# Kernel optimization log

Hardware: AMD Instinct MI355X
Metric: run time of the kernel (lower is better)

The kernel has to match this reference:

```python
import jax, jax.numpy as jnp
import numpy as np

DIM_MODEL = 2048
DQK = 64
DV = 64
NUM_HEADS = 32
NUM_GROUPS = 8
H_PER_G = NUM_HEADS // NUM_GROUPS
ROPE_THETA = 10000.0
RMS_EPS = 1e-6


def _rope(x):
    # x: [b, g, h, s, d]; rotate-half RoPE over last dim, positions along s.
    d = x.shape[-1]
    s = x.shape[-2]
    inv_freq = 1.0 / (ROPE_THETA ** (jnp.arange(0, d, 2, dtype=jnp.float32) / d))  # [d/2]
    ang = jnp.arange(s, dtype=jnp.float32)[:, None] * inv_freq[None, :]  # [s, d/2]
    cos, sin = jnp.cos(ang), jnp.sin(ang)
    x1, x2 = x[..., : d // 2], x[..., d // 2 :]
    return jnp.concatenate([x1 * cos - x2 * sin, x2 * cos + x1 * sin], axis=-1)


def setup_inputs() -> dict:
    key = jax.random.key(0)
    k1, k2, k3 = jax.random.split(key, 3)
    b, s = 2, 2048
    concat = NUM_HEADS * DQK + NUM_GROUPS * (DQK + DV)  # 3072
    x = jax.random.normal(k1, (b, s, DIM_MODEL), dtype=jnp.float32)
    w_in = jax.random.normal(k2, (concat, DIM_MODEL), dtype=jnp.float32) * (DIM_MODEL ** -0.5)
    w_out = jax.random.normal(k3, (DIM_MODEL, NUM_HEADS * DV), dtype=jnp.float32) * ((NUM_HEADS * DV) ** -0.5)
    rms_w = jnp.ones((DIM_MODEL,), dtype=jnp.float32)
    return {"x": x, "w_in": w_in, "w_out": w_out, "rms_w": rms_w}


def reference(x, w_in, w_out, rms_w):
    b, s, _ = x.shape
    # RMSNorm
    y = x * jax.lax.rsqrt(jnp.mean(x * x, axis=-1, keepdims=True) + RMS_EPS) * rms_w
    # In-projection (Linear, no bias): y @ w_in.T
    y = jnp.einsum('bsm,cm->bsc', y, w_in)
    cq = NUM_HEADS * DQK
    ck = NUM_GROUPS * DQK
    q, k, v = y[..., :cq], y[..., cq:cq + ck], y[..., cq + ck:]
    # q: b s (g h d) -> b g h s d ; k,v: b s (g d) -> b g 1 s d
    q = q.reshape(b, s, NUM_GROUPS, H_PER_G, DQK).transpose(0, 2, 3, 1, 4)
    k = k.reshape(b, s, NUM_GROUPS, DQK).transpose(0, 2, 1, 3)[:, :, None]
    v = v.reshape(b, s, NUM_GROUPS, DV).transpose(0, 2, 1, 3)[:, :, None]
    q = _rope(q)
    k = _rope(k)
    # scores with GQA broadcast over h
    qk = jnp.einsum('bghsd,bgxpd->bghsp', q, k) * (DQK ** -0.5)
    causal = jnp.tril(jnp.ones((s, s), dtype=bool))
    qk = jnp.where(causal, qk, -jnp.inf)
    attn = jax.nn.softmax(qk, axis=-1)
    o = jnp.einsum('bghsp,bgxpd->bghsd', attn, v)  # [b,g,h,s,d]
    o = o.transpose(0, 3, 1, 2, 4).reshape(b, s, NUM_HEADS * DV)
    y = jnp.einsum('bsc,mc->bsm', o, w_out)
    return x + y
```

## Files before the change

### kernel.cpp

```cpp
#include <hip/hip_runtime.h>
#include <hip/hip_bf16.h>

#define TOKENS   4096
#define SEQ      2048
#define DMODEL   2048
#define CONCAT   3072
#define NHEADS   32
#define NGROUPS  8
#define HPERG    4
#define CQ       2048
#define CK       512

typedef __attribute__((ext_vector_type(8))) short bf16x8;
typedef __attribute__((ext_vector_type(4))) float f32x4;

__device__ __forceinline__ ushort f2bf(float f) {
    __hip_bfloat16 h = __float2bfloat16(f);
    return __builtin_bit_cast(ushort, h);
}

__device__ __forceinline__ uint cvt_pk_bf16(float lo, float hi) {
    uint r;
    asm("v_cvt_pk_bf16_f32 %0, %1, %2" : "=v"(r) : "v"(lo), "v"(hi));
    return r;
}

#define GLOBAL_TO_LDS16(g, l)                                                  \
    __builtin_amdgcn_global_load_lds(                                          \
        (const __attribute__((address_space(1))) void*)(g),                    \
        (__attribute__((address_space(3))) void*)(l), 16, 0, 0)

__global__ void rmsnorm_kernel(const float* __restrict__ x,
                               const float* __restrict__ w,
                               ushort* __restrict__ y_bf) {
    int t = blockIdx.x;
    const float4* xr = (const float4*)(x + (size_t)t * DMODEL);
    float4 v[2];
    float ss = 0.f;
#pragma unroll
    for (int i = 0; i < 2; i++) {
        v[i] = xr[threadIdx.x + i * 256];
        ss += v[i].x * v[i].x + v[i].y * v[i].y + v[i].z * v[i].z + v[i].w * v[i].w;
    }
#pragma unroll
    for (int off = 32; off >= 1; off >>= 1) ss += __shfl_xor(ss, off);
    __shared__ float red[4];
    int wid = threadIdx.x >> 6;
    if ((threadIdx.x & 63) == 0) red[wid] = ss;
    __syncthreads();
    float total = red[0] + red[1] + red[2] + red[3];
    float scale = rsqrtf(total * (1.0f / DMODEL) + 1e-6f);
    const float4* wr = (const float4*)w;
    ushort4* yr = (ushort4*)(y_bf + (size_t)t * DMODEL);
#pragma unroll
    for (int i = 0; i < 2; i++) {
        int c = threadIdx.x + i * 256;
        float4 wv = wr[c];
        ushort4 o;
        o.x = f2bf(v[i].x * scale * wv.x);
        o.y = f2bf(v[i].y * scale * wv.y);
        o.z = f2bf(v[i].z * scale * wv.z);
        o.w = f2bf(v[i].w * scale * wv.w);
        yr[c] = o;
    }
}

__global__ void pack_bf16_kernel(const float* __restrict__ src,
                                 ushort* __restrict__ dst, int n4) {
    int i = blockIdx.x * 256 + threadIdx.x;
    if (i < n4) {
        float4 v = ((const float4*)src)[i];
        ushort4 o;
        o.x = f2bf(v.x); o.y = f2bf(v.y); o.z = f2bf(v.z); o.w = f2bf(v.w);
        ((ushort4*)dst)[i] = o;
    }
}

#define LGKM(nn) asm volatile("s_waitcnt lgkmcnt(" #nn ")" ::: "memory")
#define VMC(nn)  asm volatile("s_waitcnt vmcnt(" #nn ")" ::: "memory")
#define SBAR()   __builtin_amdgcn_s_barrier()
#define SCHED0() __builtin_amdgcn_sched_barrier(0)
#define PRIO(p)  __builtin_amdgcn_s_setprio(p)

#define RD_A(mh)                                                              \
    _Pragma("unroll") for (int mi = 0; mi < 4; mi++)                          \
    _Pragma("unroll") for (int ks = 0; ks < 2; ks++)                          \
        af[mi][ks] = *(const bf16x8*)(Ab +                                    \
            ((arow0 + (mh) * 64 + mi * 16) * 8 +                              \
             ((ks * 4 + quad) ^ an)) * 8);

#define RD_B(nh)                                                              \
    _Pragma("unroll") for (int ni = 0; ni < NFRAG; ni++)                      \
    _Pragma("unroll") for (int ks = 0; ks < 2; ks++)                          \
        bfr[nh][ni][ks] = *(const bf16x8*)(Bb +                               \
            ((brow0 + (nh) * (16 * NFRAG) + ni * 16) * 8 +                    \
             ((ks * 4 + quad) ^ an)) * 8);

#define MMQ(mh, nh)                                                           \
    _Pragma("unroll") for (int mi = 0; mi < 4; mi++)                          \
    _Pragma("unroll") for (int ni = 0; ni < NFRAG; ni++)                      \
    _Pragma("unroll") for (int ks = 0; ks < 2; ks++)                          \
        acc[(mh) * 4 + mi][(nh) * NFRAG + ni] =                               \
            __builtin_amdgcn_mfma_f32_16x16x32_bf16(af[mi][ks],               \
                bfr[nh][ni][ks], acc[(mh) * 4 + mi][(nh) * NFRAG + ni],       \
                0, 0, 0);

#define ISSUE_HALF(H_)                                                        \
    {                                                                         \
        int H = (H_);                                                         \
        if (H < 4 * NT) {                                                     \
            int t2 = H >> 2, j2 = H & 3;                                      \
            int k0 = t2 << 6;                                                 \
            if (j2 == 0 || j2 == 3) {                                         \
                int half = (j2 == 3);                                         \
                ushort* lb = (ushort*)&As[t2 & 1][0];                         \
                _Pragma("unroll") for (int c = 0; c < 2; c++) {               \
                    int s = w * 2 + c;                                        \
                    int row = (s >> 3) * 128 + half * 64 + (s & 7) * 8;       \
                    const ushort* g = Aptr +                                  \
                        (size_t)(bm + row + l8) * K + k0 + kb8;               \
                    GLOBAL_TO_LDS16(g, lb + row * 64);                        \
                }                                                             \
            } else {                                                          \
                int half = (j2 == 2);                                         \
                ushort* lb = (ushort*)&Bs[t2 & 1][0];                         \
                if constexpr (NFRAG == 2) {                                   \
                    _Pragma("unroll") for (int c = 0; c < 2; c++) {           \
                        int s = w * 2 + c;                                    \
                        int row = (s >> 2) * 64 + half * 32 + (s & 3) * 8;    \
                        const ushort* g = Bptr +                              \
                            (size_t)(bn + row + l8) * K + k0 + kb8;           \
                        GLOBAL_TO_LDS16(g, lb + row * 64);                    \
                    }                                                         \
                } else {                                                      \
                    int row = (w >> 1) * 32 + half * 16 + (w & 1) * 8;        \
                    const ushort* g = Bptr +                                  \
                        (size_t)(bn + row + l8) * K + k0 + kb8;               \
                    GLOBAL_TO_LDS16(g, lb + row * 64);                        \
                }                                                             \
            }                                                                 \
        }                                                                     \
    }

#define VMC_STEADY()                                                          \
    { if constexpr (NFRAG == 2) { VMC(6); } else { VMC(4); } }

#define TILE(t_, BUF)                                                         \
    {                                                                         \
        const ushort* Ab = &As[BUF][0];                                       \
        const ushort* Bb = &Bs[BUF][0];                                       \
                                                \
        RD_A(0); RD_B(0);                                                     \
        ISSUE_HALF(4 * (t_) + 7);                                             \
        LGKM(8);                                                              \
        SBAR(); LGKM(0); SCHED0();                                            \
        PRIO(1); MMQ(0, 0); PRIO(0);                                          \
        SBAR();                                                               \
                                                   \
        RD_B(1);                                                              \
        ISSUE_HALF(4 * (t_) + 8);                                             \
        SBAR(); LGKM(0); SCHED0();                                            \
        PRIO(1); MMQ(0, 1); PRIO(0);                                          \
        SBAR();                                                               \
                                                   \
        RD_A(1);                                                              \
        ISSUE_HALF(4 * (t_) + 9);                                             \
        SBAR(); LGKM(0); SCHED0();                                            \
        PRIO(1); MMQ(1, 0); PRIO(0);                                          \
        SBAR();                                                               \
                           \
        ISSUE_HALF(4 * (t_) + 10);                                            \
        SBAR(); SCHED0();                                                     \
        PRIO(1); MMQ(1, 1); PRIO(0);                                          \
        if ((t_) + 2 < NT)        { VMC_STEADY(); }                           \
        else if ((t_) + 2 == NT)  { VMC(0); }                                 \
        SBAR();                                                               \
    }

template <bool EPILOGUE, int NFRAG>
__global__ __launch_bounds__(512, 2) void gemm_nt_8ph(
        const ushort* __restrict__ Aptr, const ushort* __restrict__ Bptr,
        float* __restrict__ C, const float* __restrict__ X,
        float* __restrict__ OUT, int M, int N, int K) {
    __shared__ __align__(16) ushort As[2][256 * 64];
    __shared__ __align__(16) ushort Bs[2][NFRAG * 128 * 64];

    int nwg = (int)(gridDim.x * gridDim.y);
    int lin = (int)(blockIdx.y * gridDim.x + blockIdx.x);
    int swz = lin;
    if ((nwg & 7) == 0) swz = (lin & 7) * (nwg >> 3) + (lin >> 3);
    const int bm = (swz / (int)gridDim.x) * 256;
    const int bn = (swz % (int)gridDim.x) * (128 * NFRAG);

    const int w = threadIdx.x >> 6, lane = threadIdx.x & 63;
    const int n = lane & 15, quad = lane >> 4;
    const int wm = w >> 2, wn = w & 3;
    const int an = n & 7;
    const int l8 = lane >> 3;
    const int kb8 = ((lane & 7) ^ l8) * 8;
    const int arow0 = wm * 128 + n;
    const int brow0 = wn * (32 * NFRAG) + n;
    const int NT = K >> 6;

    f32x4 acc[8][2 * NFRAG] = {};
    bf16x8 af[4][2], bfr[2][NFRAG][2];

    ISSUE_HALF(0); ISSUE_HALF(1); ISSUE_HALF(2); ISSUE_HALF(3);
    ISSUE_HALF(4); ISSUE_HALF(5); ISSUE_HALF(6);
    VMC_STEADY();
    SBAR();

    for (int tt = 0; tt < NT; tt += 2) {
        TILE(tt, 0);
        TILE(tt + 1, 1);
    }

#pragma unroll
    for (int mi = 0; mi < 8; mi++)
#pragma unroll
        for (int ni = 0; ni < 2 * NFRAG; ni++) {
            int row = bm + wm * 128 + mi * 16 + quad * 4;
            int col = bn + wn * (32 * NFRAG) + ni * 16 + n;
#pragma unroll
            for (int r = 0; r < 4; r++) {
                size_t idx = (size_t)(row + r) * N + col;
                float v = acc[mi][ni][r];
                if (EPILOGUE) OUT[idx] = X[idx] + v;
                else          C[idx]   = v;
            }
        }
}

__global__ void pack_qkv_kernel(const float* __restrict__ qkv,
                                ushort* __restrict__ Qb,
                                ushort* __restrict__ Kb,
                                ushort* __restrict__ Vb) {
    __shared__ float cs[32], sn[32];
    __shared__ float tile[64][65];
    int tid = threadIdx.x;

    if (blockIdx.x < TOKENS) {
        int t = blockIdx.x;
        int b = t >> 11, s = t & (SEQ - 1);
        const float* row = qkv + (size_t)t * CONCAT;
        if (tid < 32) {
            const float LOG2_THETA = 13.287712379549449f;
            float inv = exp2f(-((float)tid / 32.0f) * LOG2_THETA);
            float ang = (float)s * inv;
            cs[tid] = cosf(ang);
            sn[tid] = sinf(ang);
        }
        __syncthreads();
        const float QSCALE = 0.18033688011112042f;
#pragma unroll
        for (int it = 0; it < (CQ + CK) / 2 / 256; it++) {
            int p = tid + it * 256;
            int head = p >> 5, j = p & 31;
            const float* hb = row + head * 64;
            float x1 = hb[j], x2 = hb[j + 32];
            float c = cs[j], s2 = sn[j];
            float o1 = x1 * c - x2 * s2;
            float o2 = x2 * c + x1 * s2;
            if (head < 32) {
                o1 *= QSCALE; o2 *= QSCALE;
                int g = head >> 2, h = head & 3;
                ushort* q = Qb + ((size_t)((b * 8 + g) * 4 + h) * SEQ + s) * 64;
                q[j]      = f2bf(o1);
                q[j + 32] = f2bf(o2);
            } else {
                int kh = head - 32;
                ushort* kk = Kb + ((size_t)(b * 8 + kh) * SEQ + s) * 64;
                kk[j]      = f2bf(o1);
                kk[j + 32] = f2bf(o2);
            }
        }
    } else {
        int bid = blockIdx.x - TOKENS;
        int st = bid & 31, bg = bid >> 5;
        int b = bg >> 3, g = bg & 7;
        int ls = tid >> 6;
        int d = tid & 63;
#pragma unroll
        for (int i = 0; i < 16; i++) {
            int s = st * 64 + i * 4 + ls;
            tile[i * 4 + ls][d] =
                qkv[(size_t)(b * SEQ + s) * CONCAT + CQ + CK + g * 64 + d];
        }
        __syncthreads();
#pragma unroll
        for (int i = 0; i < 16; i++) {
            int drow = i * 4 + ls;
            int scol = tid & 63;
            Vb[((size_t)(bg * 64 + drow)) * SEQ + st * 64 + scol] =
                f2bf(tile[scol][drow]);
        }
    }
}

#define AISSUE(kt_, buf_)                                                     \
    {                                                                         \
        const ushort* Kg_ = Kg0 + (kt_) * 64 * 64;                            \
        const ushort* Vg_ = Vg0 + (kt_) * 64;                                 \
        GLOBAL_TO_LDS16(Kg_ + (w * 8 + l3) * 64 + lx * 8,                     \
                        &Kl[buf_][(size_t)threadIdx.x * 8]);                  \
        GLOBAL_TO_LDS16(Vg_ + (size_t)(w * 8 + l3) * SEQ + lx * 8,            \
                        &Vl[buf_][(size_t)threadIdx.x * 8]);                  \
    }

__global__ __launch_bounds__(512) void attn_mfma_kernel(
        const ushort* __restrict__ Qb, const ushort* __restrict__ Kb,
        const ushort* __restrict__ Vb, ushort* __restrict__ o_bf) {
    __shared__ __align__(16) ushort Kl[2][512 * 8];
    __shared__ __align__(16) ushort Vl[2][512 * 8];
    __shared__ __align__(16) uint   Pl[8][544];

    int blk = blockIdx.x;
    int qt  = 15 - (blk >> 6);
    int bgh = blk & 63;
    int h = bgh & 3, g = (bgh >> 2) & 7, b = bgh >> 5;
    int w = threadIdx.x >> 6, lane = threadIdx.x & 63;
    int n = lane & 15, quad = lane >> 4;
    const int an = n & 7;
    int Q0 = qt * 128;
    int qw = Q0 + w * 16;

    const int l3 = lane >> 3;
    const int lx = (lane & 7) ^ l3;

    const ushort* Qh  = Qb + (size_t)((b * 8 + g) * 4 + h) * (SEQ * 64);
    const ushort* Kg0 = Kb + (size_t)(b * 8 + g) * (SEQ * 64);
    const ushort* Vg0 = Vb + (size_t)(b * 8 + g) * (64 * SEQ);

    bf16x8 aq[2];
#pragma unroll
    for (int ks = 0; ks < 2; ks++)
        aq[ks] = *(const bf16x8*)(
            Qh + (size_t)(qw + n) * 64 + ks * 32 + quad * 8);

    f32x4 od[4] = {};
    f32x4 od4 = {};

    short onev = (n == 0) ? (short)0x3F80 : (short)0;
    bf16x8 bones = {onev, onev, onev, onev, onev, onev, onev, onev};

    uint* Pw = Pl[w];
    int nkt = qt * 2 + 2;

    AISSUE(0, 0);
    AISSUE(1, 1);

    for (int kt = 0; kt < nkt; kt++) {
        int buf = kt & 1;
        if (kt + 1 < nkt) { VMC(2); } else { VMC(0); }
        SBAR(); SCHED0();

        bool act = (kt * 64 <= qw + 15);
        if (act) {
            const ushort* Kb_ = Kl[buf];
            const ushort* Vb_ = Vl[buf];

#pragma unroll
            for (int t16k = 0; t16k < 4; t16k++) {
                int krow = (t16k * 16 + n) * 8;
                bf16x8 kf0 = *(const bf16x8*)(Kb_ + (krow + (quad ^ an)) * 8);
                bf16x8 kf1 = *(const bf16x8*)(Kb_ + (krow + ((quad + 4) ^ an)) * 8);
                int key0 = kt * 64 + t16k * 16 + quad * 4;
                f32x4 c = {};
                PRIO(1);
                c = __builtin_amdgcn_mfma_f32_16x16x32_bf16(kf0, aq[0], c, 0, 0, 0);
                c = __builtin_amdgcn_mfma_f32_16x16x32_bf16(kf1, aq[1], c, 0, 0, 0);
                PRIO(0);
                int qrow = qw + n;
                float p[4];
                if (kt * 64 + 63 > qw) {
#pragma unroll
                    for (int r = 0; r < 4; r++)
                        p[r] = (key0 + r <= qrow) ? __builtin_amdgcn_exp2f(c[r]) : 0.f;
                } else {
#pragma unroll
                    for (int r = 0; r < 4; r++)
                        p[r] = __builtin_amdgcn_exp2f(c[r]);
                }
                uint d0 = cvt_pk_bf16(p[0], p[1]);
                uint d1 = cvt_pk_bf16(p[2], p[3]);
                int base = ((t16k * 2 + (quad >> 1)) * 17 + n) * 4
                           + (quad & 1) * 2;
                Pw[base]     = d0;
                Pw[base + 1] = d1;
            }

#pragma unroll
            for (int kb2 = 0; kb2 < 2; kb2++) {
                int kb = kb2 * 4 + quad;
                bf16x8 bv[4];
#pragma unroll
                for (int dt = 0; dt < 4; dt++)
                    bv[dt] = *(const bf16x8*)(Vb_ +
                        (((dt * 16 + n) * 8 + (kb ^ an)) * 8));
                bf16x8 ap = *(const bf16x8*)(
                    (const ushort*)Pw + ((kb2 * 4 + quad) * 17 + n) * 8);
                PRIO(1);
#pragma unroll
                for (int dt = 0; dt < 4; dt++)
                    od[dt] = __builtin_amdgcn_mfma_f32_16x16x32_bf16(
                        ap, bv[dt], od[dt], 0, 0, 0);
                od4 = __builtin_amdgcn_mfma_f32_16x16x32_bf16(
                    ap, bones, od4, 0, 0, 0);
                PRIO(0);
            }
        }

        SCHED0(); SBAR();
        if (kt + 2 < nkt) AISSUE(kt + 2, buf);
    }

    float linv[4];
#pragma unroll
    for (int r = 0; r < 4; r++) {
        float lv = __shfl(od4[r], lane & 48);
        linv[r] = __builtin_amdgcn_rcpf(lv);
    }
#pragma unroll
    for (int dt = 0; dt < 4; dt++)
#pragma unroll
        for (int r = 0; r < 4; r++) {
            int q = qw + quad * 4 + r;
            int col = (g * 4 + h) * 64 + dt * 16 + n;
            o_bf[(size_t)(b * SEQ + q) * DMODEL + col] =
                f2bf(od[dt][r] * linv[r]);
        }
}

extern "C" void kernel_launch(void* const* d_in, const int* in_sizes, int n_in,
                              void* d_out, int out_size, void* d_ws, size_t ws_size,
                              hipStream_t stream) {
    const float* x     = (const float*)d_in[0];
    const float* w_in  = (const float*)d_in[1];
    const float* w_out = (const float*)d_in[2];
    const float* rms_w = (const float*)d_in[3];
    float* out = (float*)d_out;

    const size_t MB = 1024 * 1024;
    char* ws = (char*)d_ws;
    float*  qkv      = (float*)ws;
    ushort* y_bf     = (ushort*)(ws + 48 * MB);
    ushort* w_in_bf  = (ushort*)(ws + 64 * MB);
    ushort* Qb       = (ushort*)(ws + 48 * MB);
    ushort* Kb       = (ushort*)(ws + 64 * MB);
    ushort* Vb       = (ushort*)(ws + 68 * MB);
    ushort* o_bf     = (ushort*)ws;
    ushort* w_out_bf = (ushort*)(ws + 16 * MB);

    rmsnorm_kernel<<<TOKENS, 256, 0, stream>>>(x, rms_w, y_bf);
    pack_bf16_kernel<<<(CONCAT * DMODEL / 4 + 255) / 256, 256, 0, stream>>>(
        w_in, w_in_bf, CONCAT * DMODEL / 4);

    gemm_nt_8ph<false, 2><<<dim3(CONCAT / 256, TOKENS / 256), 512, 0, stream>>>(
        y_bf, w_in_bf, qkv, nullptr, nullptr, TOKENS, CONCAT, DMODEL);

    pack_qkv_kernel<<<TOKENS + 512, 256, 0, stream>>>(
        qkv, Qb, Kb, Vb);
    pack_bf16_kernel<<<(DMODEL * DMODEL / 4 + 255) / 256, 256, 0, stream>>>(
        w_out, w_out_bf, DMODEL * DMODEL / 4);

    attn_mfma_kernel<<<1024, 512, 0, stream>>>(Qb, Kb, Vb, o_bf);

    gemm_nt_8ph<true, 1><<<dim3(DMODEL / 128, TOKENS / 256), 512, 0, stream>>>(
        o_bf, w_out_bf, nullptr, x, out, TOKENS, DMODEL, DMODEL);
}
```

Measured before the change: 290.5 us.

## Fuse RoPE, Q scaling and QKV packing into in-projection GEMM epilogue

The in-projection GEMM epilogue now applies RoPE (cos/sin tables built in reused LDS), Q scaling and bf16 conversion, and writes Q, K and transposed V directly. This removes the fp32 qkv intermediate and the separate pack_qkv pass. The two weight-conversion launches are merged into one kernel. The cost is a heavier GEMM epilogue with scattered 2-byte stores, including strided transposed V writes.

Measured after the change: 279.8 us. 1.04x faster.

```diff
diff --git a/kernel.cpp b/kernel.cpp
--- a/kernel.cpp
+++ b/kernel.cpp
@@ -65,15 +65,23 @@
     }
 }
 
-__global__ void pack_bf16_kernel(const float* __restrict__ src,
-                                 ushort* __restrict__ dst, int n4) {
+#define N4_WIN  (CONCAT * DMODEL / 4)
+#define N4_WOUT (DMODEL * DMODEL / 4)
+__global__ void pack_weights_kernel(const float* __restrict__ w_in,
+                                    const float* __restrict__ w_out,
+                                    ushort* __restrict__ w_in_bf,
+                                    ushort* __restrict__ w_out_bf) {
     int i = blockIdx.x * 256 + threadIdx.x;
-    if (i < n4) {
-        float4 v = ((const float4*)src)[i];
-        ushort4 o;
-        o.x = f2bf(v.x); o.y = f2bf(v.y); o.z = f2bf(v.z); o.w = f2bf(v.w);
-        ((ushort4*)dst)[i] = o;
-    }
+    const float* src;
+    ushort* dst;
+    int j;
+    if (i < N4_WIN) { src = w_in; dst = w_in_bf; j = i; }
+    else if (i < N4_WIN + N4_WOUT) { src = w_out; dst = w_out_bf; j = i - N4_WIN; }
+    else return;
+    float4 v = ((const float4*)src)[j];
+    ushort4 o;
+    o.x = f2bf(v.x); o.y = f2bf(v.y); o.z = f2bf(v.z); o.w = f2bf(v.w);
+    ((ushort4*)dst)[j] = o;
 }
 
 #define LGKM(nn) asm volatile("s_waitcnt lgkmcnt(" #nn ")" ::: "memory")
@@ -177,11 +185,12 @@
         SBAR();                                                               \
     }
 
-template <bool EPILOGUE, int NFRAG>
+template <int EPI, int NFRAG>
 __global__ __launch_bounds__(512, 2) void gemm_nt_8ph(
         const ushort* __restrict__ Aptr, const ushort* __restrict__ Bptr,
-        float* __restrict__ C, const float* __restrict__ X,
-        float* __restrict__ OUT, int M, int N, int K) {
+        const float* __restrict__ X, float* __restrict__ OUT,
+        ushort* __restrict__ Qb_, ushort* __restrict__ Kb_,
+        ushort* __restrict__ Vb_, int M, int N, int K) {
     __shared__ __align__(16) ushort As[2][256 * 64];
     __shared__ __align__(16) ushort Bs[2][NFRAG * 128 * 64];
 
@@ -215,85 +224,85 @@
         TILE(tt + 1, 1);
     }
 
-#pragma unroll
-    for (int mi = 0; mi < 8; mi++)
-#pragma unroll
-        for (int ni = 0; ni < 2 * NFRAG; ni++) {
-            int row = bm + wm * 128 + mi * 16 + quad * 4;
-            int col = bn + wn * (32 * NFRAG) + ni * 16 + n;
-#pragma unroll
-            for (int r = 0; r < 4; r++) {
-                size_t idx = (size_t)(row + r) * N + col;
-                float v = acc[mi][ni][r];
-                if (EPILOGUE) OUT[idx] = X[idx] + v;
-                else          C[idx]   = v;
-            }
-        }
-}
-
-__global__ void pack_qkv_kernel(const float* __restrict__ qkv,
-                                ushort* __restrict__ Qb,
-                                ushort* __restrict__ Kb,
-                                ushort* __restrict__ Vb) {
-    __shared__ float cs[32], sn[32];
-    __shared__ float tile[64][65];
-    int tid = threadIdx.x;
-
-    if (blockIdx.x < TOKENS) {
-        int t = blockIdx.x;
-        int b = t >> 11, s = t & (SEQ - 1);
-        const float* row = qkv + (size_t)t * CONCAT;
-        if (tid < 32) {
-            const float LOG2_THETA = 13.287712379549449f;
-            float inv = exp2f(-((float)tid / 32.0f) * LOG2_THETA);
-            float ang = (float)s * inv;
-            cs[tid] = cosf(ang);
-            sn[tid] = sinf(ang);
+    if constexpr (EPI == 2) {
+        float* cosT = (float*)&As[0][0];
+        float* sinT = (float*)&Bs[0][0];
+        const float LOG2_THETA = 13.287712379549449f;
+        const int bq = bm >> 11;
+        const int s0 = bm & 2047;
+#pragma unroll
+        for (int t = 0; t < 16; t++) {
+            int e = (int)threadIdx.x + t * 512;
+            int sl = e >> 5, j = e & 31;
+            float inv = exp2f(-((float)j / 32.0f) * LOG2_THETA);
+            float ang = (float)(s0 + sl) * inv;
+            cosT[sl * 37 + j] = cosf(ang);
+            sinT[sl * 37 + j] = sinf(ang);
         }
         __syncthreads();
-        const float QSCALE = 0.18033688011112042f;
-#pragma unroll
-        for (int it = 0; it < (CQ + CK) / 2 / 256; it++) {
-            int p = tid + it * 256;
-            int head = p >> 5, j = p & 31;
-            const float* hb = row + head * 64;
-            float x1 = hb[j], x2 = hb[j + 32];
-            float c = cs[j], s2 = sn[j];
-            float o1 = x1 * c - x2 * s2;
-            float o2 = x2 * c + x1 * s2;
-            if (head < 32) {
-                o1 *= QSCALE; o2 *= QSCALE;
-                int g = head >> 2, h = head & 3;
-                ushort* q = Qb + ((size_t)((b * 8 + g) * 4 + h) * SEQ + s) * 64;
-                q[j]      = f2bf(o1);
-                q[j + 32] = f2bf(o2);
+
+        int col0 = bn + wn * 64;
+        int slb = wm * 128 + quad * 4;
+        if (col0 < CQ + CK) {
+            bool isQ = col0 < CQ;
+            ushort* base;
+            if (isQ) {
+                int head = col0 >> 6;
+                int gq = head >> 2, hq = head & 3;
+                base = Qb_ + ((size_t)((bq * 8 + gq) * 4 + hq) * SEQ) * 64;
             } else {
-                int kh = head - 32;
-                ushort* kk = Kb + ((size_t)(b * 8 + kh) * SEQ + s) * 64;
-                kk[j]      = f2bf(o1);
-                kk[j + 32] = f2bf(o2);
+                int kh = (col0 - CQ) >> 6;
+                base = Kb_ + ((size_t)(bq * 8 + kh) * SEQ) * 64;
             }
+            const float QS = 0.18033688011112042f;
+#pragma unroll
+            for (int mi = 0; mi < 8; mi++)
+#pragma unroll
+                for (int r = 0; r < 4; r++) {
+                    int sl = slb + mi * 16 + r;
+                    int s = s0 + sl;
+#pragma unroll
+                    for (int jj = 0; jj < 2; jj++) {
+                        int j = jj * 16 + n;
+                        float c  = cosT[sl * 37 + j];
+                        float sv = sinT[sl * 37 + j];
+                        float x1 = acc[mi][jj][r];
+                        float x2 = acc[mi][jj + 2][r];
+                        float o1 = x1 * c - x2 * sv;
+                        float o2 = x2 * c + x1 * sv;
+                        if (isQ) { o1 *= QS; o2 *= QS; }
+                        base[(size_t)s * 64 + j]      = f2bf(o1);
+                        base[(size_t)s * 64 + j + 32] = f2bf(o2);
+                    }
+                }
+        } else {
+            int vh = (col0 - CQ - CK) >> 6;
+            ushort* base = Vb_ + (size_t)(bq * 8 + vh) * 64 * SEQ;
+#pragma unroll
+            for (int mi = 0; mi < 8; mi++)
+#pragma unroll
+                for (int ni = 0; ni < 2 * NFRAG; ni++) {
+                    int d = ni * 16 + n;
+#pragma unroll
+                    for (int r = 0; r < 4; r++) {
+                        int s = s0 + slb + mi * 16 + r;
+                        base[(size_t)d * SEQ + s] = f2bf(acc[mi][ni][r]);
+                    }
+                }
         }
     } else {
-        int bid = blockIdx.x - TOKENS;
-        int st = bid & 31, bg = bid >> 5;
-        int b = bg >> 3, g = bg & 7;
-        int ls = tid >> 6;
-        int d = tid & 63;
-#pragma unroll
-        for (int i = 0; i < 16; i++) {
-            int s = st * 64 + i * 4 + ls;
-            tile[i * 4 + ls][d] =
-                qkv[(size_t)(b * SEQ + s) * CONCAT + CQ + CK + g * 64 + d];
-        }
-        __syncthreads();
-#pragma unroll
-        for (int i = 0; i < 16; i++) {
-            int drow = i * 4 + ls;
-            int scol = tid & 63;
-            Vb[((size_t)(bg * 64 + drow)) * SEQ + st * 64 + scol] =
-                f2bf(tile[scol][drow]);
-        }
+#pragma unroll
+        for (int mi = 0; mi < 8; mi++)
+#pragma unroll
+            for (int ni = 0; ni < 2 * NFRAG; ni++) {
+                int row = bm + wm * 128 + mi * 16 + quad * 4;
+                int col = bn + wn * (32 * NFRAG) + ni * 16 + n;
+#pragma unroll
+                for (int r = 0; r < 4; r++) {
+                    size_t idx = (size_t)(row + r) * N + col;
+                    OUT[idx] = X[idx] + acc[mi][ni][r];
+                }
+            }
     }
 }
 
@@ -442,29 +451,24 @@
 
     const size_t MB = 1024 * 1024;
     char* ws = (char*)d_ws;
-    float*  qkv      = (float*)ws;
+    ushort* Qb       = (ushort*)ws;
+    ushort* Kb       = (ushort*)(ws + 16 * MB);
+    ushort* Vb       = (ushort*)(ws + 20 * MB);
+    ushort* o_bf     = (ushort*)(ws + 24 * MB);
+    ushort* w_out_bf = (ushort*)(ws + 40 * MB);
     ushort* y_bf     = (ushort*)(ws + 48 * MB);
     ushort* w_in_bf  = (ushort*)(ws + 64 * MB);
-    ushort* Qb       = (ushort*)(ws + 48 * MB);
-    ushort* Kb       = (ushort*)(ws + 64 * MB);
-    ushort* Vb       = (ushort*)(ws + 68 * MB);
-    ushort* o_bf     = (ushort*)ws;
-    ushort* w_out_bf = (ushort*)(ws + 16 * MB);
 
     rmsnorm_kernel<<<TOKENS, 256, 0, stream>>>(x, rms_w, y_bf);
-    pack_bf16_kernel<<<(CONCAT * DMODEL / 4 + 255) / 256, 256, 0, stream>>>(
-        w_in, w_in_bf, CONCAT * DMODEL / 4);
-
-    gemm_nt_8ph<false, 2><<<dim3(CONCAT / 256, TOKENS / 256), 512, 0, stream>>>(
-        y_bf, w_in_bf, qkv, nullptr, nullptr, TOKENS, CONCAT, DMODEL);
-
-    pack_qkv_kernel<<<TOKENS + 512, 256, 0, stream>>>(
-        qkv, Qb, Kb, Vb);
-    pack_bf16_kernel<<<(DMODEL * DMODEL / 4 + 255) / 256, 256, 0, stream>>>(
-        w_out, w_out_bf, DMODEL * DMODEL / 4);
+    pack_weights_kernel<<<(N4_WIN + N4_WOUT + 255) / 256, 256, 0, stream>>>(
+        w_in, w_out, w_in_bf, w_out_bf);
+
+    gemm_nt_8ph<2, 2><<<dim3(CONCAT / 256, TOKENS / 256), 512, 0, stream>>>(
+        y_bf, w_in_bf, nullptr, nullptr, Qb, Kb, Vb, TOKENS, CONCAT, DMODEL);
 
     attn_mfma_kernel<<<1024, 512, 0, stream>>>(Qb, Kb, Vb, o_bf);
 
-    gemm_nt_8ph<true, 1><<<dim3(DMODEL / 128, TOKENS / 256), 512, 0, stream>>>(
-        o_bf, w_out_bf, nullptr, x, out, TOKENS, DMODEL, DMODEL);
-}
+    gemm_nt_8ph<1, 1><<<dim3(DMODEL / 128, TOKENS / 256), 512, 0, stream>>>(
+        o_bf, w_out_bf, x, out, nullptr, nullptr, nullptr,
+        TOKENS, DMODEL, DMODEL);
+}
```
